# Performance work log

Hardware: AMD Instinct MI355X
Metric: run time of the kernel (lower is better)

## Reference

```python
import jax, jax.numpy as jnp
from jax import lax
import numpy as np


def setup_inputs() -> dict:
    key = jax.random.key(0)
    encode_image = jax.random.normal(key, (32, 3, 512, 512), dtype=jnp.float32)
    return {"encode_image": encode_image, "w": 5}


def _box_blur(x, w):
    # cv2.blur with ksize (w, w): normalized box filter, BORDER_REFLECT_101 padding.
    # Implemented as a separable depthwise convolution (two 1D average passes).
    B, C, H, W = x.shape
    p = w // 2  # w is odd -> symmetric padding, matches cv2 default anchor
    xp = jnp.pad(x, ((0, 0), (0, 0), (p, p), (p, p)), mode="reflect")  # REFLECT_101
    kh = jnp.full((C, 1, w, 1), 1.0 / w, dtype=x.dtype)  # vertical pass
    kw = jnp.full((C, 1, 1, w), 1.0 / w, dtype=x.dtype)  # horizontal pass
    dn = ("NCHW", "OIHW", "NCHW")
    y = lax.conv_general_dilated(xp, kh, (1, 1), "VALID",
                                 dimension_numbers=dn, feature_group_count=C)
    y = lax.conv_general_dilated(y, kw, (1, 1), "VALID",
                                 dimension_numbers=dn, feature_group_count=C)
    return y  # (B, C, H, W)


def reference(encode_image, w):
    # Faithful to Smooth.forward: replaces noise_and_cover[0] with the box-blurred
    # image; we return the blurred tensor (the only modified element).
    return _box_blur(encode_image, w)
```

## Files before the change

kernel.cpp:

```cpp
#include <hip/hip_runtime.h>


#define WID 512
#define HEI 512
#define RPT 16
#define TXN 16
#define TYN 16

__device__ __forceinline__ float4 add4(float4 a, float4 b) {
    return make_float4(a.x + b.x, a.y + b.y, a.z + b.z, a.w + b.w);
}
__device__ __forceinline__ float4 sub4(float4 a, float4 b) {
    return make_float4(a.x - b.x, a.y - b.y, a.z - b.z, a.w - b.w);
}

__global__ __launch_bounds__(256) void smooth_box5_kernel(
    const float* __restrict__ in, float* __restrict__ out)
{
    const int tid = threadIdx.x;
    const int tx  = tid & (TXN - 1);
    const int ty  = tid >> 4;
    const int c   = blockIdx.x * (TXN * 4) + tx * 4;
    const int r0  = blockIdx.y * (TYN * RPT) + ty * RPT;
    const long long plane = blockIdx.z;

    const float* __restrict__ ip = in  + plane * (long long)(HEI * WID);
    float*       __restrict__ op = out + plane * (long long)(HEI * WID);

    const bool leftE  = (c == 0);
    const bool rightE = (c == WID - 4);

    auto hsum = [&](int gy) -> float4 {
        gy = (gy < 0) ? -gy : ((gy >= HEI) ? (2 * HEI - 2 - gy) : gy);
        const float* row = ip + gy * WID;
        float4 m = *reinterpret_cast<const float4*>(row + c);
        float2 l, r;
        if (leftE)  l = make_float2(m.z, m.y);
        else        l = *reinterpret_cast<const float2*>(row + c - 2);
        if (rightE) r = make_float2(m.z, m.y);
        else        r = *reinterpret_cast<const float2*>(row + c + 4);
        float t  = m.y + m.z;
        float u  = m.x + t;
        float v  = t + m.w;
        float s4 = u + m.w;
        float4 h;
        h.x = (l.x + l.y) + u;
        h.y = l.y + s4;
        h.z = s4 + r.x;
        h.w = v + (r.x + r.y);
        return h;
    };

    float4 h[5];
    h[0] = hsum(r0 - 2);
    h[1] = hsum(r0 - 1);
    h[2] = hsum(r0);
    h[3] = hsum(r0 + 1);
    float4 vs = add4(add4(h[0], h[1]), add4(h[2], h[3]));

    float* orow = op + r0 * WID + c;

    #pragma unroll
    for (int k = 0; k < RPT; ++k) {
        float4 hn = hsum(r0 + 2 + k);
        h[(4 + k) % 5] = hn;
        vs = add4(vs, hn);
        float4 o = make_float4(vs.x * 0.04f, vs.y * 0.04f,
                               vs.z * 0.04f, vs.w * 0.04f);
        *reinterpret_cast<float4*>(orow) = o;
        vs = sub4(vs, h[k % 5]);
        orow += WID;
    }
}

extern "C" void kernel_launch(void* const* d_in, const int* in_sizes, int n_in,
                              void* d_out, int out_size, void* d_ws, size_t ws_size,
                              hipStream_t stream) {
    const float* img = (const float*)d_in[0];
    float* out = (float*)d_out;
    const int B = 32, C = 3;
    dim3 grid(WID / (TXN * 4), HEI / (TYN * RPT), B * C);
    dim3 block(256);
    smooth_box5_kernel<<<grid, block, 0, stream>>>(img, out);
}
```

Before: 197.7 us.

## Map full rows to wavefronts and fetch horizontal halos via lane shuffles

Each 64-lane wavefront now covers a full 512-wide row at 8 floats per lane and processes 8 rows. Horizontal halo values come from neighbouring lanes through shuffles instead of extra float2 global loads. The next row is also prefetched one iteration ahead. This cuts redundant halo loads but shortens the per-thread vertical run, so proportionally more overlapping rows are reloaded, and it adds cross-lane shuffle cost.

```diff
diff --git a/kernel.cpp b/kernel.cpp
--- a/kernel.cpp
+++ b/kernel.cpp
@@ -3,72 +3,86 @@
 
 #define WID 512
 #define HEI 512
-#define RPT 16
-#define TXN 16
-#define TYN 16
-
-__device__ __forceinline__ float4 add4(float4 a, float4 b) {
-    return make_float4(a.x + b.x, a.y + b.y, a.z + b.z, a.w + b.w);
-}
-__device__ __forceinline__ float4 sub4(float4 a, float4 b) {
-    return make_float4(a.x - b.x, a.y - b.y, a.z - b.z, a.w - b.w);
-}
+#define RPT 8
+#define STRIP (4 * RPT)
 
 __global__ __launch_bounds__(256) void smooth_box5_kernel(
     const float* __restrict__ in, float* __restrict__ out)
 {
-    const int tid = threadIdx.x;
-    const int tx  = tid & (TXN - 1);
-    const int ty  = tid >> 4;
-    const int c   = blockIdx.x * (TXN * 4) + tx * 4;
-    const int r0  = blockIdx.y * (TYN * RPT) + ty * RPT;
-    const long long plane = blockIdx.z;
+    const int tid  = threadIdx.x;
+    const int lane = tid & 63;
+    const int wv   = tid >> 6;
+    const int c    = lane << 3;
+    const int r0   = blockIdx.x * STRIP + wv * RPT;
+    const long long plane = blockIdx.y;
 
     const float* __restrict__ ip = in  + plane * (long long)(HEI * WID);
     float*       __restrict__ op = out + plane * (long long)(HEI * WID);
 
-    const bool leftE  = (c == 0);
-    const bool rightE = (c == WID - 4);
+    const bool Ledge = (lane == 0);
+    const bool Redge = (lane == 63);
 
-    auto hsum = [&](int gy) -> float4 {
+    auto loadraw = [&](int gy, float4& m0, float4& m1) {
         gy = (gy < 0) ? -gy : ((gy >= HEI) ? (2 * HEI - 2 - gy) : gy);
-        const float* row = ip + gy * WID;
-        float4 m = *reinterpret_cast<const float4*>(row + c);
-        float2 l, r;
-        if (leftE)  l = make_float2(m.z, m.y);
-        else        l = *reinterpret_cast<const float2*>(row + c - 2);
-        if (rightE) r = make_float2(m.z, m.y);
-        else        r = *reinterpret_cast<const float2*>(row + c + 4);
-        float t  = m.y + m.z;
-        float u  = m.x + t;
-        float v  = t + m.w;
-        float s4 = u + m.w;
-        float4 h;
-        h.x = (l.x + l.y) + u;
-        h.y = l.y + s4;
-        h.z = s4 + r.x;
-        h.w = v + (r.x + r.y);
-        return h;
+        const float* row = ip + gy * WID + c;
+        m0 = *reinterpret_cast<const float4*>(row);
+        m1 = *reinterpret_cast<const float4*>(row + 4);
     };
 
-    float4 h[5];
-    h[0] = hsum(r0 - 2);
-    h[1] = hsum(r0 - 1);
-    h[2] = hsum(r0);
-    h[3] = hsum(r0 + 1);
-    float4 vs = add4(add4(h[0], h[1]), add4(h[2], h[3]));
+    auto hsum = [&](const float4 m0, const float4 m1, float h[8]) {
+        float lx = __shfl_up(m1.z, 1);
+        float ly = __shfl_up(m1.w, 1);
+        float rx = __shfl_down(m0.x, 1);
+        float ry = __shfl_down(m0.y, 1);
+        if (Ledge) { lx = m0.z; ly = m0.y; }
+        if (Redge) { rx = m1.z; ry = m1.y; }
+        float a[12] = { lx, ly, m0.x, m0.y, m0.z, m0.w,
+                        m1.x, m1.y, m1.z, m1.w, rx, ry };
+        float t[11];
+        #pragma unroll
+        for (int j = 0; j < 11; ++j) t[j] = a[j] + a[j + 1];
+        #pragma unroll
+        for (int j = 0; j < 8; ++j) h[j] = t[j] + t[j + 2] + a[j + 4];
+    };
 
-    float* orow = op + r0 * WID + c;
+    float h[5][8];
+    float vs[8];
+    float4 cm0, cm1, nm0, nm1;
+
+    loadraw(r0 - 2, cm0, cm1);
+    loadraw(r0 - 1, nm0, nm1);
+    hsum(cm0, cm1, h[0]);
+    cm0 = nm0; cm1 = nm1; loadraw(r0,     nm0, nm1);
+    hsum(cm0, cm1, h[1]);
+    cm0 = nm0; cm1 = nm1; loadraw(r0 + 1, nm0, nm1);
+    hsum(cm0, cm1, h[2]);
+    cm0 = nm0; cm1 = nm1; loadraw(r0 + 2, nm0, nm1);
+    hsum(cm0, cm1, h[3]);
+
+    #pragma unroll
+    for (int j = 0; j < 8; ++j)
+        vs[j] = h[0][j] + h[1][j] + h[2][j] + h[3][j];
+
+    float* orow = op + (long long)r0 * WID + c;
 
     #pragma unroll
     for (int k = 0; k < RPT; ++k) {
-        float4 hn = hsum(r0 + 2 + k);
-        h[(4 + k) % 5] = hn;
-        vs = add4(vs, hn);
-        float4 o = make_float4(vs.x * 0.04f, vs.y * 0.04f,
-                               vs.z * 0.04f, vs.w * 0.04f);
-        *reinterpret_cast<float4*>(orow) = o;
-        vs = sub4(vs, h[k % 5]);
+        cm0 = nm0; cm1 = nm1;
+        if (k < RPT - 1) loadraw(r0 + 3 + k, nm0, nm1);
+        float hn[8];
+        hsum(cm0, cm1, hn);
+        #pragma unroll
+        for (int j = 0; j < 8; ++j) h[(4 + k) % 5][j] = hn[j];
+        float o[8];
+        #pragma unroll
+        for (int j = 0; j < 8; ++j) {
+            vs[j] += hn[j];
+            o[j] = vs[j] * 0.04f;
+        }
+        *reinterpret_cast<float4*>(orow)     = make_float4(o[0], o[1], o[2], o[3]);
+        *reinterpret_cast<float4*>(orow + 4) = make_float4(o[4], o[5], o[6], o[7]);
+        #pragma unroll
+        for (int j = 0; j < 8; ++j) vs[j] -= h[k % 5][j];
         orow += WID;
     }
 }
@@ -79,7 +93,7 @@
     const float* img = (const float*)d_in[0];
     float* out = (float*)d_out;
     const int B = 32, C = 3;
-    dim3 grid(WID / (TXN * 4), HEI / (TYN * RPT), B * C);
+    dim3 grid(HEI / STRIP, B * C);
     dim3 block(256);
     smooth_box5_kernel<<<grid, block, 0, stream>>>(img, out);
 }
```

Measured after the change: 189.5 us. 4.2% less time.
